# Kernel tuning notes

Hardware: AMD Instinct MI355X
Metric: run time of the kernel (lower is better)

Reference implementation:

```python
import jax, jax.numpy as jnp
import numpy as np

N_NODES = 20000
N_EDGES = 320000
IN_CH = 512
HID = 128
HEADS = 4
OUT_CH = 30
NEG_SLOPE = 0.2  # PyG GATConv default negative_slope


def add_self_loops(ei, n):
    loops = jnp.arange(n, dtype=ei.dtype)
    return jnp.concatenate([ei, jnp.stack([loops, loops])], axis=1)


def gat_layer(x, ei, W, a_src, a_dst, b, concat):
    # x: [N, F_in], ei: [2, E] (source row 0 -> target row 1), W: [F_in, H*C]
    n = x.shape[0]
    H, C = a_src.shape
    h = (x @ W).reshape(n, H, C)                      # [N, H, C]
    src, dst = ei[0], ei[1]
    al_src = jnp.einsum('nhc,hc->nh', h, a_src)       # [N, H]
    al_dst = jnp.einsum('nhc,hc->nh', h, a_dst)
    e = al_src[src] + al_dst[dst]                     # [E, H]
    e = jnp.where(e > 0, e, NEG_SLOPE * e)            # LeakyReLU
    # segment softmax over destination nodes (stable)
    emax = jax.lax.stop_gradient(jax.ops.segment_max(e, dst, num_segments=n))
    p = jnp.exp(e - emax[dst])
    denom = jax.ops.segment_sum(p, dst, num_segments=n)
    alpha = p / denom[dst]                            # [E, H]
    msg = h[src] * alpha[:, :, None]                  # [E, H, C]
    out = jax.ops.segment_sum(msg, dst, num_segments=n)  # [N, H, C]
    out = out.reshape(n, H * C) if concat else out.mean(axis=1)
    return out + b


def setup_inputs() -> dict:
    key = jax.random.key(0)
    ks = jax.random.split(key, 12)
    s = 0.05
    x = jax.random.normal(ks[0], (N_NODES, IN_CH), jnp.float32)
    edge_index = jax.random.randint(ks[1], (2, N_EDGES), 0, N_NODES, jnp.int32)
    return {
        'x': x,
        'edge_index': edge_index,
        'W1': jax.random.normal(ks[2], (IN_CH, HEADS * HID), jnp.float32) * s,
        'a_src1': jax.random.normal(ks[3], (HEADS, HID), jnp.float32) * s,
        'a_dst1': jax.random.normal(ks[4], (HEADS, HID), jnp.float32) * s,
        'b1': jnp.zeros((HEADS * HID,), jnp.float32),
        'W2': jax.random.normal(ks[5], (HEADS * HID, OUT_CH), jnp.float32) * s,
        'a_src2': jax.random.normal(ks[6], (1, OUT_CH), jnp.float32) * s,
        'a_dst2': jax.random.normal(ks[7], (1, OUT_CH), jnp.float32) * s,
        'b2': jnp.zeros((OUT_CH,), jnp.float32),
        'Wd': jax.random.normal(ks[8], (OUT_CH, IN_CH), jnp.float32) * s,
        'bd': jnp.zeros((IN_CH,), jnp.float32),
    }


def reference(x, edge_index, W1, a_src1, a_dst1, b1, W2, a_src2, a_dst2, b2, Wd, bd):
    n = x.shape[0]
    ei = add_self_loops(edge_index, n)
    h = gat_layer(x, ei, W1, a_src1, a_dst1, b1, concat=True)   # [N, HEADS*HID]
    h = jax.nn.elu(h)                                           # dropout is identity in eval
    z = gat_layer(h, ei, W2, a_src2, a_dst2, b2, concat=False)  # [N, OUT_CH]
    x_hat = z @ Wd + bd                                         # [N, IN_CH]
    return (x_hat, z)
```

## Files before the change

kernel.cpp:

```cpp
#include <hip/hip_runtime.h>
#include <hip/hip_bf16.h>
#include <stdint.h>

#define N_NODES 20000
#define N_EDGES 320000
#define IN_CH 512
#define HID 128
#define HEADS 4
#define HC 512
#define OUT_CH 30
#define NEG_SLOPE 0.2f
#define M_PAD 20096
#define PARTS 79
#define CAST_BLOCKS (M_PAD * IN_CH / 4 / 256)
#define G1_BLOCKS (M_PAD / 128 * 4)
#define CNT_BLOCKS (N_EDGES / 256)

typedef _Float16 half8 __attribute__((ext_vector_type(8)));
typedef _Float16 half4v __attribute__((ext_vector_type(4)));
typedef float f32x4 __attribute__((ext_vector_type(4)));

static __device__ __forceinline__ float lrelu(float e) { return e > 0.f ? e : NEG_SLOPE * e; }

static __device__ __forceinline__ void gload16(const void* gsrc, void* ldst) {
  __builtin_amdgcn_global_load_lds(
      (const __attribute__((address_space(1))) uint32_t*)gsrc,
      (__attribute__((address_space(3))) uint32_t*)ldst,
      16, 0, 0);
}

__global__ __launch_bounds__(256) void k_front(const float* __restrict__ x,
                                               const float* __restrict__ W1,
                                               const float* __restrict__ W2,
                                               _Float16* __restrict__ xh,
                                               _Float16* __restrict__ W1t,
                                               _Float16* __restrict__ w2t,
                                               int* __restrict__ cnt) {
  __shared__ float t[64][65];
  const int b = blockIdx.x;
  const int tid = threadIdx.x;
  if (b < CAST_BLOCKS) {
    int i = b * 256 + tid;
    if (i < N_NODES) cnt[i] = 0;
    int base = i * 4;
    int row = base >> 9;
    half4v o;
    if (row < N_NODES) {
      float4 v = *(const float4*)(x + (size_t)base);
      o[0] = (_Float16)v.x; o[1] = (_Float16)v.y; o[2] = (_Float16)v.z; o[3] = (_Float16)v.w;
    } else {
      o[0] = o[1] = o[2] = o[3] = (_Float16)0.f;
    }
    *(half4v*)(xh + (size_t)base) = o;
  } else if (b < CAST_BLOCKS + 64) {
    const int bb = b - CAST_BLOCKS;
    const int bk = (bb & 7) * 64;
    const int bn = (bb >> 3) * 64;
#pragma unroll
    for (int it = 0; it < 16; it++) {
      int idx = tid + it * 256;
      int r = idx >> 6, c = idx & 63;
      t[r][c] = W1[(size_t)(bk + r) * HC + bn + c];
    }
    __syncthreads();
#pragma unroll
    for (int it = 0; it < 16; it++) {
      int idx = tid + it * 256;
      int rn = idx >> 6, ck = idx & 63;
      W1t[(size_t)(bn + rn) * IN_CH + bk + ck] = (_Float16)t[ck][rn];
    }
  } else {
    int idx = (b - CAST_BLOCKS - 64) * 256 + tid;
    int n = idx >> 9, k = idx & 511;
    w2t[idx] = (n < OUT_CH) ? (_Float16)W2[(size_t)k * OUT_CH + n] : (_Float16)0.f;
  }
}

__global__ __launch_bounds__(256) void k_gemm1_mfma(const _Float16* __restrict__ A,
                                                    const _Float16* __restrict__ Bt,
                                                    _Float16* __restrict__ C,
                                                    const float* __restrict__ a_src,
                                                    const float* __restrict__ a_dst,
                                                    float* __restrict__ al_s,
                                                    float* __restrict__ al_d,
                                                    const int* __restrict__ dst,
                                                    int* __restrict__ cnt) {
  __shared__ _Float16 smem[128 * 136];
  const int bx = blockIdx.x;
  const int tid = threadIdx.x;
  if (bx >= G1_BLOCKS) {
    int e = (bx - G1_BLOCKS) * 256 + tid;
    if (e < N_EDGES) atomicAdd(&cnt[dst[e]], 1);
    return;
  }
  _Float16* As = smem;
  _Float16* Bs = smem + 128 * 64;
  _Float16* Cs = smem;
  const int lane = tid & 63;
  const int w = tid >> 6;
  const int bm = (bx >> 2) * 128;
  const int head = bx & 3;
  const int bn = head * 128;

  const int lrow = lane >> 3;
  const int schunk = (lane & 7) ^ lrow;

  const int wm = w >> 1, wn = w & 1;
  const int r15 = lane & 15;
  const int q = lane >> 4;
  const int a_row0 = wm * 64 + r15;
  const int b_row0 = wn * 64 + r15;

  f32x4 acc[4][4];
  const f32x4 zero = {0.f, 0.f, 0.f, 0.f};
#pragma unroll
  for (int i = 0; i < 4; i++)
#pragma unroll
    for (int j = 0; j < 4; j++) acc[i][j] = zero;

  for (int kb = 0; kb < 8; kb++) {
    const int kof = kb * 64 + schunk * 8;
#pragma unroll
    for (int t = 0; t < 4; t++) {
      const int row = w * 32 + t * 8;
      gload16(A + (size_t)(bm + row + lrow) * IN_CH + kof, (void*)(As + row * 64));
      gload16(Bt + (size_t)(bn + row + lrow) * IN_CH + kof, (void*)(Bs + row * 64));
    }
    __syncthreads();
#pragma unroll
    for (int s = 0; s < 2; s++) {
      const int cs = ((s * 4 + q) ^ (lane & 7)) * 8;
      half8 af[4], bf[4];
#pragma unroll
      for (int i = 0; i < 4; i++) af[i] = *(const half8*)&As[(a_row0 + i * 16) * 64 + cs];
#pragma unroll
      for (int j = 0; j < 4; j++) bf[j] = *(const half8*)&Bs[(b_row0 + j * 16) * 64 + cs];
#pragma unroll
      for (int i = 0; i < 4; i++)
#pragma unroll
        for (int j = 0; j < 4; j++)
          acc[i][j] = __builtin_amdgcn_mfma_f32_16x16x32_f16(af[i], bf[j], acc[i][j], 0, 0, 0);
    }
    __syncthreads();
  }
#pragma unroll
  for (int i = 0; i < 4; i++)
#pragma unroll
    for (int j = 0; j < 4; j++)
#pragma unroll
      for (int r = 0; r < 4; r++) {
        const int row = wm * 64 + i * 16 + q * 4 + r;
        const int col = wn * 64 + j * 16 + r15;
        Cs[row * 136 + col] = (_Float16)acc[i][j][r];
      }
  __syncthreads();
#pragma unroll
  for (int it = 0; it < 8; it++) {
    int cidx = tid + it * 256;
    int row = cidx >> 4, c16 = cidx & 15;
    int gm = bm + row;
    if (gm < N_NODES)
      *(half8*)(C + (size_t)gm * HC + bn + c16 * 8) = *(const half8*)&Cs[row * 136 + c16 * 8];
  }
  const int row = tid >> 1;
  const int hf = tid & 1;
  const float* asp = a_src + head * HID + hf * 64;
  const float* adp = a_dst + head * HID + hf * 64;
  float s = 0.f, d = 0.f;
#pragma unroll
  for (int j8 = 0; j8 < 8; j8++) {
    half8 cv = *(const half8*)&Cs[row * 136 + hf * 64 + j8 * 8];
    float4 a0 = *(const float4*)(asp + j8 * 8);
    float4 a1 = *(const float4*)(asp + j8 * 8 + 4);
    float4 d0 = *(const float4*)(adp + j8 * 8);
    float4 d1 = *(const float4*)(adp + j8 * 8 + 4);
    float c0 = (float)cv[0], c1 = (float)cv[1], c2 = (float)cv[2], c3 = (float)cv[3];
    float c4 = (float)cv[4], c5 = (float)cv[5], c6 = (float)cv[6], c7 = (float)cv[7];
    s += c0 * a0.x + c1 * a0.y + c2 * a0.z + c3 * a0.w +
         c4 * a1.x + c5 * a1.y + c6 * a1.z + c7 * a1.w;
    d += c0 * d0.x + c1 * d0.y + c2 * d0.z + c3 * d0.w +
         c4 * d1.x + c5 * d1.y + c6 * d1.z + c7 * d1.w;
  }
  s += __shfl_xor(s, 1);
  d += __shfl_xor(d, 1);
  const int gm = bm + row;
  if (hf == 0 && gm < N_NODES) {
    al_s[gm * HEADS + head] = s;
    al_d[gm * HEADS + head] = d;
  }
}

__global__ __launch_bounds__(256) void k_scan_part(const int* __restrict__ cnt,
                                                   int* __restrict__ part) {
  __shared__ int ws[4];
  int i = blockIdx.x * 256 + threadIdx.x;
  int v = (i < N_NODES) ? cnt[i] : 0;
  int lane = threadIdx.x & 63;
#pragma unroll
  for (int off = 32; off; off >>= 1) v += __shfl_down(v, off);
  if (lane == 0) ws[threadIdx.x >> 6] = v;
  __syncthreads();
  if (threadIdx.x == 0) part[blockIdx.x] = ws[0] + ws[1] + ws[2] + ws[3];
}
__global__ __launch_bounds__(256) void k_scan_final(const int* __restrict__ cnt,
                                                    const int* __restrict__ part,
                                                    int* __restrict__ offs,
                                                    int* __restrict__ cursor) {
  __shared__ int buf[256];
  __shared__ int s_prefix;
  const int b = blockIdx.x;
  const int t = threadIdx.x;
  if (t < 64) {
    int v = 0;
    for (int j = t; j < b; j += 64) v += part[j];
#pragma unroll
    for (int off = 32; off; off >>= 1) v += __shfl_down(v, off);
    if (t == 0) s_prefix = v;
  }
  int i = b * 256 + t;
  int v = (i < N_NODES) ? cnt[i] : 0;
  buf[t] = v;
  __syncthreads();
#pragma unroll
  for (int off = 1; off < 256; off <<= 1) {
    int x = (t >= off) ? buf[t - off] : 0;
    __syncthreads();
    buf[t] += x;
    __syncthreads();
  }
  if (i < N_NODES) {
    int ex = s_prefix + buf[t] - v;
    offs[i] = ex;
    cursor[i] = ex;
  }
  if (b == PARTS - 1 && t == 255) offs[N_NODES] = s_prefix + buf[255];
}
__global__ void k_scatter(const int* __restrict__ src, const int* __restrict__ dst,
                          int* __restrict__ cursor, int* __restrict__ srcs) {
  int e = blockIdx.x * blockDim.x + threadIdx.x;
  if (e < N_EDGES) {
    int pos = atomicAdd(&cursor[dst[e]], 1);
    srcs[pos] = src[e];
  }
}

__global__ __launch_bounds__(256) void k_agg1(const _Float16* __restrict__ h,
                                              const float* __restrict__ al_s,
                                              const float* __restrict__ al_d,
                                              const int* __restrict__ offs,
                                              const int* __restrict__ srcs,
                                              const float* __restrict__ b1,
                                              _Float16* __restrict__ hm) {
  __shared__ __align__(16) int2 s_sp[4][64];
  const int tid = threadIdx.x;
  const int lane = tid & 63;
  const int wv = tid >> 6;
  const int qq = lane >> 4;
  const int l16 = lane & 15;
  const int head = blockIdx.x / 1250;
  const int n = (blockIdx.x % 1250) * 16 + wv * 4 + qq;
  const int cb = head * HID + l16 * 8;

  const float adn = al_d[n * HEADS + head];
  const float pself = __expf(lrelu(al_s[n * HEADS + head] + adn));

  half8 hv = *(const half8*)(h + (size_t)n * HC + cb);
  float acc[8];
  float den = pself;
#pragma unroll
  for (int j = 0; j < 8; j++) acc[j] = pself * (float)hv[j];

  const int beg = offs[n];
  const int cnt = offs[n + 1] - beg;
  int mx = cnt;
  mx = max(mx, __shfl_xor(mx, 16));
  mx = max(mx, __shfl_xor(mx, 32));

  for (int base = 0; base < mx; base += 16) {
    int sreg = n;
    float preg = 0.f;
    if (base + l16 < cnt) {
      sreg = srcs[beg + base + l16];
      preg = __expf(lrelu(al_s[sreg * HEADS + head] + adn));
    }
    s_sp[wv][lane] = make_int2(sreg, __float_as_int(preg));
    __builtin_amdgcn_wave_barrier();
    const int rem = cnt - base;
    const int m4 = rem > 16 ? 16 : ((rem + 3) & ~3);
    for (int k = 0; k < m4; k += 4) {
      int4 w0 = *(const int4*)&s_sp[wv][qq * 16 + k];
      int4 w1 = *(const int4*)&s_sp[wv][qq * 16 + k + 2];
      half8 v0 = *(const half8*)(h + (size_t)w0.x * HC + cb);
      half8 v1 = *(const half8*)(h + (size_t)w0.z * HC + cb);
      half8 v2 = *(const half8*)(h + (size_t)w1.x * HC + cb);
      half8 v3 = *(const half8*)(h + (size_t)w1.z * HC + cb);
      float p0 = __int_as_float(w0.y), p1 = __int_as_float(w0.w);
      float p2 = __int_as_float(w1.y), p3 = __int_as_float(w1.w);
      den += p0 + p1 + p2 + p3;
#pragma unroll
      for (int j = 0; j < 8; j++)
        acc[j] += p0 * (float)v0[j] + p1 * (float)v1[j] +
                  p2 * (float)v2[j] + p3 * (float)v3[j];
    }
    __builtin_amdgcn_wave_barrier();
  }
  const float inv = 1.f / den;
  float4 bb0 = *(const float4*)(b1 + cb);
  float4 bb1 = *(const float4*)(b1 + cb + 4);
  float ob[8] = {bb0.x, bb0.y, bb0.z, bb0.w, bb1.x, bb1.y, bb1.z, bb1.w};
  half8 ov;
#pragma unroll
  for (int j = 0; j < 8; j++) {
    float o = acc[j] * inv + ob[j];
    o = o > 0.f ? o : __expf(o) - 1.f;
    ov[j] = (_Float16)o;
  }
  *(half8*)(hm + (size_t)n * HC + cb) = ov;
}

__global__ __launch_bounds__(256) void k_gemm2_mfma(const _Float16* __restrict__ hm,
                                                    const _Float16* __restrict__ w2t,
                                                    const float* __restrict__ a_s2,
                                                    const float* __restrict__ a_d2,
                                                    float* __restrict__ zpre,
                                                    float* __restrict__ al_s2,
                                                    float* __restrict__ al_d2) {
  __shared__ _Float16 Bs[32 * 520];
  __shared__ _Float16 As[64 * 136];
  const int tid = threadIdx.x;
  const int lane = tid & 63;
  const int w = tid >> 6;
  const int bm = blockIdx.x * 64;
  const int n15 = lane & 15;
  const int q = lane >> 4;

#pragma unroll
  for (int it = 0; it < 8; it++) {
    int idx = (tid + it * 256) * 8;
    int n = idx >> 9, k = idx & 511;
    *(half8*)&Bs[n * 520 + k] = *(const half8*)(w2t + idx);
  }

  f32x4 acc0 = {0.f, 0.f, 0.f, 0.f}, acc1 = {0.f, 0.f, 0.f, 0.f};
  for (int kt = 0; kt < HC; kt += 128) {
#pragma unroll
    for (int p = 0; p < 4; p++) {
      int row = (tid >> 4) + p * 16;
      int kof = (tid & 15) * 8;
      int gm = bm + row;
      half8 v = {};
      if (gm < N_NODES) v = *(const half8*)(hm + (size_t)gm * HC + kt + kof);
      *(half8*)&As[row * 136 + kof] = v;
    }
    __syncthreads();
#pragma unroll
    for (int ks = 0; ks < 128; ks += 32) {
      half8 af = *(const half8*)&As[(w * 16 + n15) * 136 + ks + q * 8];
      half8 b0 = *(const half8*)&Bs[n15 * 520 + kt + ks + q * 8];
      half8 b1 = *(const half8*)&Bs[(16 + n15) * 520 + kt + ks + q * 8];
      acc0 = __builtin_amdgcn_mfma_f32_16x16x32_f16(af, b0, acc0, 0, 0, 0);
      acc1 = __builtin_amdgcn_mfma_f32_16x16x32_f16(af, b1, acc1, 0, 0, 0);
    }
    __syncthreads();
  }
  const float asn0 = (n15 < OUT_CH) ? a_s2[n15] : 0.f;
  const float asn1 = (n15 + 16 < OUT_CH) ? a_s2[n15 + 16] : 0.f;
  const float adn0 = (n15 < OUT_CH) ? a_d2[n15] : 0.f;
  const float adn1 = (n15 + 16 < OUT_CH) ? a_d2[n15 + 16] : 0.f;
#pragma unroll
  for (int r = 0; r < 4; r++) {
    const int gm = bm + w * 16 + q * 4 + r;
    const bool ok = gm < N_NODES;
    if (ok) {
      zpre[(size_t)gm * OUT_CH + n15] = acc0[r];
      if (n15 + 16 < OUT_CH) zpre[(size_t)gm * OUT_CH + n15 + 16] = acc1[r];
    }
    float s = acc0[r] * asn0 + acc1[r] * asn1;
    float d = acc0[r] * adn0 + acc1[r] * adn1;
#pragma unroll
    for (int off = 8; off; off >>= 1) {
      s += __shfl_xor(s, off);
      d += __shfl_xor(d, off);
    }
    if (n15 == 0 && ok) {
      al_s2[gm] = s;
      al_d2[gm] = d;
    }
  }
}

__global__ __launch_bounds__(256) void k_agg2(const float* __restrict__ zpre,
                                              const float* __restrict__ al_s2,
                                              const float* __restrict__ al_d2,
                                              const int* __restrict__ offs,
                                              const int* __restrict__ srcs,
                                              const float* __restrict__ b2,
                                              float* __restrict__ zout) {
  __shared__ __align__(16) int2 s_sp[4][64];
  const int tid = threadIdx.x;
  const int lane = tid & 63;
  const int wv = tid >> 6;
  const int hh = lane >> 5;
  const int l32 = lane & 31;
  const int n = blockIdx.x * 8 + wv * 2 + hh;
  const float ad2n = al_d2[n];
  const float pself = __expf(lrelu(al_s2[n] + ad2n));
  const bool act = l32 < OUT_CH;
  float zv = act ? zpre[(size_t)n * OUT_CH + l32] : 0.f;
  float acc = pself * zv;
  float den = pself;

  const int beg = offs[n];
  const int cnt = offs[n + 1] - beg;
  int mx = max(cnt, __shfl_xor(cnt, 32));

  for (int base = 0; base < mx; base += 32) {
    int sreg = n;
    float preg = 0.f;
    if (base + l32 < cnt) {
      sreg = srcs[beg + base + l32];
      preg = __expf(lrelu(al_s2[sreg] + ad2n));
    }
    s_sp[wv][lane] = make_int2(sreg, __float_as_int(preg));
    __builtin_amdgcn_wave_barrier();
    const int rem = cnt - base;
    const int m4 = rem > 32 ? 32 : ((rem + 3) & ~3);
    for (int k = 0; k < m4; k += 4) {
      int4 w0 = *(const int4*)&s_sp[wv][hh * 32 + k];
      int4 w1 = *(const int4*)&s_sp[wv][hh * 32 + k + 2];
      float v0 = act ? zpre[(size_t)w0.x * OUT_CH + l32] : 0.f;
      float v1 = act ? zpre[(size_t)w0.z * OUT_CH + l32] : 0.f;
      float v2 = act ? zpre[(size_t)w1.x * OUT_CH + l32] : 0.f;
      float v3 = act ? zpre[(size_t)w1.z * OUT_CH + l32] : 0.f;
      float p0 = __int_as_float(w0.y), p1 = __int_as_float(w0.w);
      float p2 = __int_as_float(w1.y), p3 = __int_as_float(w1.w);
      den += p0 + p1 + p2 + p3;
      acc += p0 * v0 + p1 * v1 + p2 * v2 + p3 * v3;
    }
    __builtin_amdgcn_wave_barrier();
  }
  if (act) zout[(size_t)n * OUT_CH + l32] = acc / den + b2[l32];
}

__global__ __launch_bounds__(256) void k_dec(const float* __restrict__ z,
                                             const float* __restrict__ Wd,
                                             const float* __restrict__ bd,
                                             float* __restrict__ xhat) {
  __shared__ float zs[64][32];
  const int tid = threadIdx.x;
  const int c = blockIdx.y * 256 + tid;
  float wd[32];
#pragma unroll
  for (int k = 0; k < OUT_CH; k++) wd[k] = Wd[(size_t)k * IN_CH + c];
  wd[30] = wd[31] = 0.f;
  const int n0 = blockIdx.x * 64;
  for (int idx = tid; idx < 64 * 32; idx += 256) {
    int r = idx >> 5, cc = idx & 31;
    int row = n0 + r;
    zs[r][cc] = (cc < OUT_CH && row < N_NODES) ? z[(size_t)row * OUT_CH + cc] : 0.f;
  }
  __syncthreads();
  const float b0 = bd[c];
  for (int i = 0; i < 64; i++) {
    int row = n0 + i;
    if (row >= N_NODES) break;
    float a0 = b0;
#pragma unroll
    for (int k4 = 0; k4 < 8; k4++) {
      float4 zv = *(const float4*)&zs[i][k4 * 4];
      a0 += zv.x * wd[k4 * 4 + 0] + zv.y * wd[k4 * 4 + 1] +
            zv.z * wd[k4 * 4 + 2] + zv.w * wd[k4 * 4 + 3];
    }
    xhat[(size_t)row * IN_CH + c] = a0;
  }
}

extern "C" void kernel_launch(void* const* d_in, const int* in_sizes, int n_in,
                              void* d_out, int out_size, void* d_ws, size_t ws_size,
                              hipStream_t stream) {
  const float* x    = (const float*)d_in[0];
  const int*   ei   = (const int*)d_in[1];
  const float* W1   = (const float*)d_in[2];
  const float* a_s1 = (const float*)d_in[3];
  const float* a_d1 = (const float*)d_in[4];
  const float* b1   = (const float*)d_in[5];
  const float* W2   = (const float*)d_in[6];
  const float* a_s2 = (const float*)d_in[7];
  const float* a_d2 = (const float*)d_in[8];
  const float* b2   = (const float*)d_in[9];
  const float* Wd   = (const float*)d_in[10];
  const float* bd   = (const float*)d_in[11];

  float* xhat = (float*)d_out;
  float* zout = xhat + (size_t)N_NODES * IN_CH;

  const int* srcv = ei;
  const int* dstv = ei + N_EDGES;

  char* w = (char*)d_ws;
  auto alloc = [&](size_t bytes) {
    void* p = (void*)w;
    w += (bytes + 255) & ~(size_t)255;
    return p;
  };
  _Float16* xh   = (_Float16*)alloc((size_t)M_PAD * IN_CH * 2);
  _Float16* w1t  = (_Float16*)alloc((size_t)HC * IN_CH * 2);
  _Float16* w2t  = (_Float16*)alloc((size_t)32 * HC * 2);
  _Float16* h    = (_Float16*)alloc((size_t)N_NODES * HC * 2);
  _Float16* hm   = (_Float16*)alloc((size_t)N_NODES * HC * 2);
  float* zpre  = (float*)alloc((size_t)N_NODES * OUT_CH * 4);
  float* al_s1v= (float*)alloc((size_t)N_NODES * HEADS * 4);
  float* al_d1v= (float*)alloc((size_t)N_NODES * HEADS * 4);
  float* al_s2v= (float*)alloc((size_t)N_NODES * 4);
  float* al_d2v= (float*)alloc((size_t)N_NODES * 4);
  int*   cnt   = (int*)alloc((size_t)N_NODES * 4);
  int*   offs  = (int*)alloc((size_t)(N_NODES + 1) * 4);
  int*   cursor= (int*)alloc((size_t)N_NODES * 4);
  int*   srcs  = (int*)alloc((size_t)N_EDGES * 4);
  int*   part  = (int*)alloc((size_t)PARTS * 4);

  const int EB = (N_EDGES + 255) / 256;

  k_front<<<CAST_BLOCKS + 128, 256, 0, stream>>>(x, W1, W2, xh, w1t, w2t, cnt);
  k_gemm1_mfma<<<G1_BLOCKS + CNT_BLOCKS, 256, 0, stream>>>(xh, w1t, h, a_s1, a_d1,
                                                           al_s1v, al_d1v, dstv, cnt);
  k_scan_part<<<PARTS, 256, 0, stream>>>(cnt, part);
  k_scan_final<<<PARTS, 256, 0, stream>>>(cnt, part, offs, cursor);
  k_scatter<<<EB, 256, 0, stream>>>(srcv, dstv, cursor, srcs);
  k_agg1<<<1250 * HEADS, 256, 0, stream>>>(h, al_s1v, al_d1v, offs, srcs, b1, hm);
  k_gemm2_mfma<<<(N_NODES + 63) / 64, 256, 0, stream>>>(hm, w2t, a_s2, a_d2, zpre,
                                                        al_s2v, al_d2v);
  k_agg2<<<N_NODES / 8, 256, 0, stream>>>(zpre, al_s2v, al_d2v, offs, srcs, b2, zout);
  k_dec<<<dim3((N_NODES + 63) / 64, 2), 256, 0, stream>>>(zout, Wd, bd, xhat);
}
```

Baseline: 256.8 us.

## Double-buffer GEMM1 LDS tiles and put edge-count blocks first

The first-layer MFMA GEMM now uses two LDS buffers, so it can issue the async global-to-LDS loads for the next K tile before computing on the current one, with explicit vmcnt waits and raw barriers replacing __syncthreads. The edge-degree counting blocks are moved to the front of the grid so they are scheduled before the GEMM tiles. LDS per block grows from about 34KB to 64KB, which may lower occupancy. The partial vmcnt(8) wait relies on each thread issuing exactly 8 loads per stage.

```diff
diff --git a/kernel.cpp b/kernel.cpp
--- a/kernel.cpp
+++ b/kernel.cpp
@@ -85,21 +85,20 @@
                                                     float* __restrict__ al_d,
                                                     const int* __restrict__ dst,
                                                     int* __restrict__ cnt) {
-  __shared__ _Float16 smem[128 * 136];
+  __shared__ _Float16 smem[4 * 128 * 64];
   const int bx = blockIdx.x;
   const int tid = threadIdx.x;
-  if (bx >= G1_BLOCKS) {
-    int e = (bx - G1_BLOCKS) * 256 + tid;
+  if (bx < CNT_BLOCKS) {
+    int e = bx * 256 + tid;
     if (e < N_EDGES) atomicAdd(&cnt[dst[e]], 1);
     return;
   }
-  _Float16* As = smem;
-  _Float16* Bs = smem + 128 * 64;
+  const int gbx = bx - CNT_BLOCKS;
   _Float16* Cs = smem;
   const int lane = tid & 63;
   const int w = tid >> 6;
-  const int bm = (bx >> 2) * 128;
-  const int head = bx & 3;
+  const int bm = (gbx >> 2) * 128;
+  const int head = gbx & 3;
   const int bn = head * 128;
 
   const int lrow = lane >> 3;
@@ -118,15 +117,32 @@
 #pragma unroll
     for (int j = 0; j < 4; j++) acc[i][j] = zero;
 
-  for (int kb = 0; kb < 8; kb++) {
+  auto stage = [&](int kb, int buf) {
     const int kof = kb * 64 + schunk * 8;
+    _Float16* As = smem + buf * (2 * 128 * 64);
+    _Float16* Bs = As + 128 * 64;
 #pragma unroll
     for (int t = 0; t < 4; t++) {
       const int row = w * 32 + t * 8;
       gload16(A + (size_t)(bm + row + lrow) * IN_CH + kof, (void*)(As + row * 64));
       gload16(Bt + (size_t)(bn + row + lrow) * IN_CH + kof, (void*)(Bs + row * 64));
     }
-    __syncthreads();
+  };
+
+  stage(0, 0);
+  for (int kb = 0; kb < 8; kb++) {
+    const int buf = kb & 1;
+    if (kb < 7) {
+      stage(kb + 1, buf ^ 1);
+      asm volatile("s_waitcnt vmcnt(8)" ::: "memory");
+    } else {
+      asm volatile("s_waitcnt vmcnt(0)" ::: "memory");
+    }
+    __builtin_amdgcn_sched_barrier(0);
+    __builtin_amdgcn_s_barrier();
+    __builtin_amdgcn_sched_barrier(0);
+    const _Float16* As = smem + buf * (2 * 128 * 64);
+    const _Float16* Bs = As + 128 * 64;
 #pragma unroll
     for (int s = 0; s < 2; s++) {
       const int cs = ((s * 4 + q) ^ (lane & 7)) * 8;
@@ -141,7 +157,8 @@
         for (int j = 0; j < 4; j++)
           acc[i][j] = __builtin_amdgcn_mfma_f32_16x16x32_f16(af[i], bf[j], acc[i][j], 0, 0, 0);
     }
-    __syncthreads();
+    __builtin_amdgcn_sched_barrier(0);
+    __builtin_amdgcn_s_barrier();
   }
 #pragma unroll
   for (int i = 0; i < 4; i++)
```

Result: no change. 256.4 us (-0.2%).

## Remap agg1 to 8 lanes per node over half-heads; schedule count blocks first

Applied to the files above, without the earlier changes.

The layer-1 aggregation kernel now gives each node 8 lanes covering 64 channels (half a head) instead of 16 lanes covering a full head. That puts 8 nodes in each wave and splits the grid into head-halves. Source offsets are precomputed as element offsets into a padded per-node shared array, removing a multiply in the gather loop. The edge-count atomics are moved to the front of the fused GEMM1 grid so they start early and do not tail behind the GEMM blocks. The trade-off is that twice as many lanes load edge indices and compute the exp weights per head, since each half-head block recomputes them.

```diff
diff --git a/kernel.cpp b/kernel.cpp
--- a/kernel.cpp
+++ b/kernel.cpp
@@ -88,18 +88,19 @@
   __shared__ _Float16 smem[128 * 136];
   const int bx = blockIdx.x;
   const int tid = threadIdx.x;
-  if (bx >= G1_BLOCKS) {
-    int e = (bx - G1_BLOCKS) * 256 + tid;
-    if (e < N_EDGES) atomicAdd(&cnt[dst[e]], 1);
+  if (bx < CNT_BLOCKS) {
+    int e = bx * 256 + tid;
+    atomicAdd(&cnt[dst[e]], 1);
     return;
   }
+  const int gbx = bx - CNT_BLOCKS;
   _Float16* As = smem;
   _Float16* Bs = smem + 128 * 64;
   _Float16* Cs = smem;
   const int lane = tid & 63;
   const int w = tid >> 6;
-  const int bm = (bx >> 2) * 128;
-  const int head = bx & 3;
+  const int bm = (gbx >> 2) * 128;
+  const int head = gbx & 3;
   const int bn = head * 128;
 
   const int lrow = lane >> 3;
@@ -251,15 +252,16 @@
                                               const int* __restrict__ srcs,
                                               const float* __restrict__ b1,
                                               _Float16* __restrict__ hm) {
-  __shared__ __align__(16) int2 s_sp[4][64];
+  __shared__ __align__(16) int2 s_sp[4][8][18];
   const int tid = threadIdx.x;
   const int lane = tid & 63;
   const int wv = tid >> 6;
-  const int qq = lane >> 4;
-  const int l16 = lane & 15;
-  const int head = blockIdx.x / 1250;
-  const int n = (blockIdx.x % 1250) * 16 + wv * 4 + qq;
-  const int cb = head * HID + l16 * 8;
+  const int oc = lane >> 3;
+  const int l8 = lane & 7;
+  const int hp = blockIdx.x / 625;
+  const int head = hp >> 1;
+  const int n = (blockIdx.x % 625) * 32 + wv * 8 + oc;
+  const int cb = head * HID + (hp & 1) * 64 + l8 * 8;
 
   const float adn = al_d[n * HEADS + head];
   const float pself = __expf(lrelu(al_s[n * HEADS + head] + adn));
@@ -273,27 +275,34 @@
   const int beg = offs[n];
   const int cnt = offs[n + 1] - beg;
   int mx = cnt;
+  mx = max(mx, __shfl_xor(mx, 8));
   mx = max(mx, __shfl_xor(mx, 16));
   mx = max(mx, __shfl_xor(mx, 32));
 
+  const int nself = n * HC;
   for (int base = 0; base < mx; base += 16) {
-    int sreg = n;
-    float preg = 0.f;
-    if (base + l16 < cnt) {
-      sreg = srcs[beg + base + l16];
-      preg = __expf(lrelu(al_s[sreg * HEADS + head] + adn));
-    }
-    s_sp[wv][lane] = make_int2(sreg, __float_as_int(preg));
+#pragma unroll
+    for (int t = 0; t < 2; t++) {
+      int idx = base + t * 8 + l8;
+      int soff = nself;
+      float preg = 0.f;
+      if (idx < cnt) {
+        int sreg = srcs[beg + idx];
+        soff = sreg << 9;
+        preg = __expf(lrelu(al_s[sreg * HEADS + head] + adn));
+      }
+      s_sp[wv][oc][t * 8 + l8] = make_int2(soff, __float_as_int(preg));
+    }
     __builtin_amdgcn_wave_barrier();
     const int rem = cnt - base;
     const int m4 = rem > 16 ? 16 : ((rem + 3) & ~3);
     for (int k = 0; k < m4; k += 4) {
-      int4 w0 = *(const int4*)&s_sp[wv][qq * 16 + k];
-      int4 w1 = *(const int4*)&s_sp[wv][qq * 16 + k + 2];
-      half8 v0 = *(const half8*)(h + (size_t)w0.x * HC + cb);
-      half8 v1 = *(const half8*)(h + (size_t)w0.z * HC + cb);
-      half8 v2 = *(const half8*)(h + (size_t)w1.x * HC + cb);
-      half8 v3 = *(const half8*)(h + (size_t)w1.z * HC + cb);
+      int4 w0 = *(const int4*)&s_sp[wv][oc][k];
+      int4 w1 = *(const int4*)&s_sp[wv][oc][k + 2];
+      half8 v0 = *(const half8*)(h + (size_t)(w0.x + cb));
+      half8 v1 = *(const half8*)(h + (size_t)(w0.z + cb));
+      half8 v2 = *(const half8*)(h + (size_t)(w1.x + cb));
+      half8 v3 = *(const half8*)(h + (size_t)(w1.z + cb));
       float p0 = __int_as_float(w0.y), p1 = __int_as_float(w0.w);
       float p2 = __int_as_float(w1.y), p3 = __int_as_float(w1.w);
       den += p0 + p1 + p2 + p3;
@@ -527,7 +536,7 @@
   k_scan_part<<<PARTS, 256, 0, stream>>>(cnt, part);
   k_scan_final<<<PARTS, 256, 0, stream>>>(cnt, part, offs, cursor);
   k_scatter<<<EB, 256, 0, stream>>>(srcv, dstv, cursor, srcs);
-  k_agg1<<<1250 * HEADS, 256, 0, stream>>>(h, al_s1v, al_d1v, offs, srcs, b1, hm);
+  k_agg1<<<625 * 8, 256, 0, stream>>>(h, al_s1v, al_d1v, offs, srcs, b1, hm);
   k_gemm2_mfma<<<(N_NODES + 63) / 64, 256, 0, stream>>>(hm, w2t, a_s2, a_d2, zpre,
                                                         al_s2v, al_d2v);
   k_agg2<<<N_NODES / 8, 256, 0, stream>>>(zpre, al_s2v, al_d2v, offs, srcs, b2, zout);
```

Result: slower. 265.5 us (+3.4%).

## Shrink GEMM1 tile to 64x128 with one row strip per wave

Applied to the files above, without the earlier changes.

Cuts the first-layer GEMM block tile from 128x128 to 64x128. Each wave now computes a 16-row strip across all 128 columns, so it holds 8 accumulators instead of 16 and grid size doubles. This lowers register and LDS pressure for higher occupancy and spreads work across more CUs. The cost is that each B tile is reloaded for every 64 rows, and the epilogue reduction now uses four threads per row. The edge-count bounds check was also dropped, which is safe because the edge count divides evenly by 256.

```diff
diff --git a/kernel.cpp b/kernel.cpp
--- a/kernel.cpp
+++ b/kernel.cpp
@@ -13,7 +13,7 @@
 #define M_PAD 20096
 #define PARTS 79
 #define CAST_BLOCKS (M_PAD * IN_CH / 4 / 256)
-#define G1_BLOCKS (M_PAD / 128 * 4)
+#define G1_BLOCKS (M_PAD / 64 * 4)
 #define CNT_BLOCKS (N_EDGES / 256)
 
 typedef _Float16 half8 __attribute__((ext_vector_type(8)));
@@ -85,91 +85,83 @@
                                                     float* __restrict__ al_d,
                                                     const int* __restrict__ dst,
                                                     int* __restrict__ cnt) {
-  __shared__ _Float16 smem[128 * 136];
+  __shared__ _Float16 smem[64 * 64 + 128 * 64];
   const int bx = blockIdx.x;
   const int tid = threadIdx.x;
   if (bx >= G1_BLOCKS) {
     int e = (bx - G1_BLOCKS) * 256 + tid;
-    if (e < N_EDGES) atomicAdd(&cnt[dst[e]], 1);
+    atomicAdd(&cnt[dst[e]], 1);
     return;
   }
   _Float16* As = smem;
-  _Float16* Bs = smem + 128 * 64;
+  _Float16* Bs = smem + 64 * 64;
   _Float16* Cs = smem;
   const int lane = tid & 63;
   const int w = tid >> 6;
-  const int bm = (bx >> 2) * 128;
+  const int bm = (bx >> 2) * 64;
   const int head = bx & 3;
   const int bn = head * 128;
 
   const int lrow = lane >> 3;
   const int schunk = (lane & 7) ^ lrow;
-
-  const int wm = w >> 1, wn = w & 1;
   const int r15 = lane & 15;
   const int q = lane >> 4;
-  const int a_row0 = wm * 64 + r15;
-  const int b_row0 = wn * 64 + r15;
-
-  f32x4 acc[4][4];
+
+  f32x4 acc[8];
   const f32x4 zero = {0.f, 0.f, 0.f, 0.f};
 #pragma unroll
-  for (int i = 0; i < 4; i++)
-#pragma unroll
-    for (int j = 0; j < 4; j++) acc[i][j] = zero;
+  for (int j = 0; j < 8; j++) acc[j] = zero;
 
   for (int kb = 0; kb < 8; kb++) {
     const int kof = kb * 64 + schunk * 8;
 #pragma unroll
+    for (int t = 0; t < 2; t++) {
+      const int row = w * 16 + t * 8;
+      gload16(A + (size_t)(bm + row + lrow) * IN_CH + kof, (void*)(As + row * 64));
+    }
+#pragma unroll
     for (int t = 0; t < 4; t++) {
       const int row = w * 32 + t * 8;
-      gload16(A + (size_t)(bm + row + lrow) * IN_CH + kof, (void*)(As + row * 64));
       gload16(Bt + (size_t)(bn + row + lrow) * IN_CH + kof, (void*)(Bs + row * 64));
     }
     __syncthreads();
 #pragma unroll
     for (int s = 0; s < 2; s++) {
       const int cs = ((s * 4 + q) ^ (lane & 7)) * 8;
-      half8 af[4], bf[4];
-#pragma unroll
-      for (int i = 0; i < 4; i++) af[i] = *(const half8*)&As[(a_row0 + i * 16) * 64 + cs];
-#pragma unroll
-      for (int j = 0; j < 4; j++) bf[j] = *(const half8*)&Bs[(b_row0 + j * 16) * 64 + cs];
-#pragma unroll
-      for (int i = 0; i < 4; i++)
-#pragma unroll
-        for (int j = 0; j < 4; j++)
-          acc[i][j] = __builtin_amdgcn_mfma_f32_16x16x32_f16(af[i], bf[j], acc[i][j], 0, 0, 0);
-    }
-    __syncthreads();
-  }
-#pragma unroll
-  for (int i = 0; i < 4; i++)
-#pragma unroll
-    for (int j = 0; j < 4; j++)
-#pragma unroll
-      for (int r = 0; r < 4; r++) {
-        const int row = wm * 64 + i * 16 + q * 4 + r;
-        const int col = wn * 64 + j * 16 + r15;
-        Cs[row * 136 + col] = (_Float16)acc[i][j][r];
+      half8 af = *(const half8*)&As[(w * 16 + r15) * 64 + cs];
+#pragma unroll
+      for (int j = 0; j < 8; j++) {
+        half8 bf = *(const half8*)&Bs[(j * 16 + r15) * 64 + cs];
+        acc[j] = __builtin_amdgcn_mfma_f32_16x16x32_f16(af, bf, acc[j], 0, 0, 0);
       }
+    }
+    __syncthreads();
+  }
+#pragma unroll
+  for (int j = 0; j < 8; j++)
+#pragma unroll
+    for (int r = 0; r < 4; r++) {
+      const int row = w * 16 + q * 4 + r;
+      const int col = j * 16 + r15;
+      Cs[row * 136 + col] = (_Float16)acc[j][r];
+    }
   __syncthreads();
 #pragma unroll
-  for (int it = 0; it < 8; it++) {
+  for (int it = 0; it < 4; it++) {
     int cidx = tid + it * 256;
     int row = cidx >> 4, c16 = cidx & 15;
     int gm = bm + row;
     if (gm < N_NODES)
       *(half8*)(C + (size_t)gm * HC + bn + c16 * 8) = *(const half8*)&Cs[row * 136 + c16 * 8];
   }
-  const int row = tid >> 1;
-  const int hf = tid & 1;
-  const float* asp = a_src + head * HID + hf * 64;
-  const float* adp = a_dst + head * HID + hf * 64;
+  const int row = tid >> 2;
+  const int qr = tid & 3;
+  const float* asp = a_src + head * HID + qr * 32;
+  const float* adp = a_dst + head * HID + qr * 32;
   float s = 0.f, d = 0.f;
 #pragma unroll
-  for (int j8 = 0; j8 < 8; j8++) {
-    half8 cv = *(const half8*)&Cs[row * 136 + hf * 64 + j8 * 8];
+  for (int j8 = 0; j8 < 4; j8++) {
+    half8 cv = *(const half8*)&Cs[row * 136 + qr * 32 + j8 * 8];
     float4 a0 = *(const float4*)(asp + j8 * 8);
     float4 a1 = *(const float4*)(asp + j8 * 8 + 4);
     float4 d0 = *(const float4*)(adp + j8 * 8);
@@ -182,9 +174,11 @@
          c4 * d1.x + c5 * d1.y + c6 * d1.z + c7 * d1.w;
   }
   s += __shfl_xor(s, 1);
+  s += __shfl_xor(s, 2);
   d += __shfl_xor(d, 1);
+  d += __shfl_xor(d, 2);
   const int gm = bm + row;
-  if (hf == 0 && gm < N_NODES) {
+  if (qr == 0 && gm < N_NODES) {
     al_s[gm * HEADS + head] = s;
     al_d[gm * HEADS + head] = d;
   }
```

Measured after the change: 259.8 us. About the same (+1.1%).
